# Kernel tuning notes

Hardware: AMD Instinct MI355X
Metric: run time of the kernel (lower is better)

Reference implementation:

```python
import jax, jax.numpy as jnp
import numpy as np

B, N, F, FH, H = 8, 2048, 64, 64, 4
NEG_BIG = -1e10


def setup_inputs() -> dict:
    key = jax.random.key(0)
    k_x, k_a, k_w, k_as, k_an = jax.random.split(key, 5)
    X = jax.random.normal(k_x, (B, N, F), dtype=jnp.float32)
    A = (jax.random.uniform(k_a, (B, N, N)) < 0.1).astype(jnp.float32)
    A = jnp.maximum(A, jnp.eye(N, dtype=jnp.float32)[None])
    W = jax.random.normal(k_w, (H, F, FH), dtype=jnp.float32) * (1.0 / np.sqrt(F))
    b = jnp.zeros((H, FH), dtype=jnp.float32)
    a_self = jax.random.normal(k_as, (H, FH), dtype=jnp.float32) * (1.0 / np.sqrt(FH))
    a_neigh = jax.random.normal(k_an, (H, FH), dtype=jnp.float32) * (1.0 / np.sqrt(FH))
    return {"X": X, "A": A, "W": W, "b": b, "a_self": a_self, "a_neigh": a_neigh}


def reference(X, A, W, b, a_self, a_neigh):
    # per-head linear projection: [B,H,N,FH]
    feats = jnp.einsum("bnf,hfo->bhno", X, W)
    # additive attention logits: e_ij = leaky_relu(a_s.h_i + a_n.h_j)
    s_self = jnp.einsum("bhno,ho->bhn", feats, a_self)   # [B,H,N]
    s_neigh = jnp.einsum("bhno,ho->bhn", feats, a_neigh)  # [B,H,N]
    scores = s_self[:, :, :, None] + s_neigh[:, :, None, :]  # [B,H,N,N]
    scores = jax.nn.leaky_relu(scores, negative_slope=0.2)
    scores = scores + (1.0 - A)[:, None] * NEG_BIG  # adjacency mask
    attn = jax.nn.softmax(scores, axis=-1)
    # weighted aggregation + bias (dropouts are identity at inference)
    out = jnp.einsum("bhnm,bhmo->bhno", attn, feats) + b[None, :, None, :]
    # concat heads -> [B,N,H*FH], then activation
    Bd, Hd, Nd, Fd = out.shape
    out = jnp.transpose(out, (0, 2, 1, 3)).reshape(Bd, Nd, Hd * Fd)
    return jax.nn.relu(out)
```

## Files before the change

### kernel.cpp

```cpp
#include <hip/hip_runtime.h>
#include <hip/hip_bf16.h>
#include <stdint.h>

#define B_ 8
#define N_ 2048
#define F_ 64
#define FH_ 64
#define H_ 4
#define C_ (H_*FH_)
#define CHUNK 64
#define NCHUNK (N_/CHUNK)
#define LOG2E 1.44269504088896340736f

typedef short short8 __attribute__((ext_vector_type(8)));
typedef float f32x4 __attribute__((ext_vector_type(4)));

__device__ __forceinline__ short f2bf(float f) {
    __hip_bfloat16 h = __float2bfloat16(f);
    return __builtin_bit_cast(short, h);
}

__global__ __launch_bounds__(256) void kf(const float* __restrict__ A,
                                          const float* __restrict__ X,
                                          const float* __restrict__ W,
                                          const float* __restrict__ a_self,
                                          const float* __restrict__ a_neigh,
                                          unsigned long long* __restrict__ Amask,
                                          __hip_bfloat16* __restrict__ featsT,
                                          float* __restrict__ ss,
                                          float* __restrict__ sn) {
    __shared__ float a_lds[2][FH_];
    __shared__ __hip_bfloat16 cw_lds[FH_ * 72];
    const int bx = blockIdx.x;
    const int tid = threadIdx.x;
    const int wave = tid >> 6, lane = tid & 63;

    if (bx >= 1024) {
        const int R = (bx - 1024) * 4 + wave;
        const float* arow = A + (size_t)R * N_;
        unsigned long long* mrow = Amask + (size_t)R * (N_ / 64);
#pragma unroll
        for (int i = 0; i < 8; ++i) {
            float a0 = arow[i * 256 + lane];
            float a1 = arow[i * 256 + 64 + lane];
            float a2 = arow[i * 256 + 128 + lane];
            float a3 = arow[i * 256 + 192 + lane];
            unsigned long long m0 = __ballot(a0 != 0.0f);
            unsigned long long m1 = __ballot(a1 != 0.0f);
            unsigned long long m2 = __ballot(a2 != 0.0f);
            unsigned long long m3 = __ballot(a3 != 0.0f);
            if (lane == 0) {
                mrow[i * 4 + 0] = m0; mrow[i * 4 + 1] = m1;
                mrow[i * 4 + 2] = m2; mrow[i * 4 + 3] = m3;
            }
        }
        return;
    }

    const int nb = bx & 31, h = (bx >> 5) & 3, b = bx >> 7;

    if (tid < 64)       a_lds[0][tid] = a_self[h * FH_ + tid];
    else if (tid < 128) a_lds[1][tid - 64] = a_neigh[h * FH_ + tid - 64];
    {
        int f = tid >> 2, o0 = (tid & 3) * 16;
        const float* wsrc = W + ((size_t)(h * F_ + f)) * FH_ + o0;
#pragma unroll
        for (int k = 0; k < 16; ++k)
            cw_lds[(o0 + k) * 72 + f] = __float2bfloat16(wsrc[k]);
    }
    __syncthreads();

    const int m = lane & 15, q = lane >> 4;
    const int nl = wave * 16 + m;
    const int n = nb * 64 + nl;
    f32x4 acc[4] = {};
#pragma unroll
    for (int ks = 0; ks < 2; ++ks) {
        const float* xp = X + ((size_t)(b * N_ + n)) * F_ + ks * 32 + q * 8;
        float4 x0 = *(const float4*)xp;
        float4 x1 = *(const float4*)(xp + 4);
        short8 bfrag;
        bfrag[0] = f2bf(x0.x); bfrag[1] = f2bf(x0.y);
        bfrag[2] = f2bf(x0.z); bfrag[3] = f2bf(x0.w);
        bfrag[4] = f2bf(x1.x); bfrag[5] = f2bf(x1.y);
        bfrag[6] = f2bf(x1.z); bfrag[7] = f2bf(x1.w);
#pragma unroll
        for (int ot = 0; ot < 4; ++ot) {
            short8 afrag = *(const short8*)(cw_lds + (ot * 16 + m) * 72 + ks * 32 + q * 8);
            acc[ot] = __builtin_amdgcn_mfma_f32_16x16x32_bf16(afrag, bfrag, acc[ot], 0, 0, 0);
        }
    }
    __syncthreads();
    float ssv = 0.f, snv = 0.f;
#pragma unroll
    for (int ot = 0; ot < 4; ++ot) {
#pragma unroll
        for (int r = 0; r < 4; ++r) {
            int orow = ot * 16 + q * 4 + r;
            float v = acc[ot][r];
            cw_lds[orow * 72 + nl] = __float2bfloat16(v);
            ssv += v * a_lds[0][orow];
            snv += v * a_lds[1][orow];
        }
    }
    ssv += __shfl_xor(ssv, 16); ssv += __shfl_xor(ssv, 32);
    snv += __shfl_xor(snv, 16); snv += __shfl_xor(snv, 32);
    __syncthreads();
    {
        int o = tid >> 2, c = (tid & 3) * 16;
        const __hip_bfloat16* src = cw_lds + o * 72 + c;
        __hip_bfloat16* dst = featsT + ((size_t)(b * H_ + h) * FH_ + o) * N_ + nb * 64 + c;
        *(uint4*)dst       = *(const uint4*)src;
        *(uint4*)(dst + 8) = *(const uint4*)(src + 8);
    }
    if (lane < 16) {
        size_t idx = ((size_t)(b * H_ + h)) * N_ + n;
        ss[idx] = ssv * LOG2E;
        sn[idx] = snv * LOG2E;
    }
}

__global__ __launch_bounds__(256) void k3_attn(const unsigned int* __restrict__ Amask,
                                               const __hip_bfloat16* __restrict__ featsT,
                                               const float* __restrict__ ss,
                                               const float* __restrict__ sn,
                                               const float* __restrict__ bias,
                                               float* __restrict__ out) {
    __shared__ float e1_lds[N_];
    __shared__ float e2_lds[N_];

    const int tile = blockIdx.x, h = blockIdx.y, b = blockIdx.z;
    const int tid = threadIdx.x, wave = tid >> 6, lane = tid & 63;
    const int m = lane & 15, q = lane >> 4;
    const int wavebase = tile * 128 + wave * 32;

    {
        const float4* snrow = (const float4*)(sn + ((size_t)(b * H_ + h)) * N_);
        float4* e1v = (float4*)e1_lds;
        float4* e2v = (float4*)e2_lds;
#pragma unroll
        for (int i = 0; i < 2; ++i) {
            int idx = tid + i * 256;
            float4 v = snrow[idx];
            float4 u1, u2;
            u1.x = exp2f(v.x); u1.y = exp2f(v.y); u1.z = exp2f(v.z); u1.w = exp2f(v.w);
            u2.x = exp2f(0.2f * v.x); u2.y = exp2f(0.2f * v.y);
            u2.z = exp2f(0.2f * v.z); u2.w = exp2f(0.2f * v.w);
            e1v[idx] = u1; e2v[idx] = u2;
        }
    }
    const float* ssrow = ss + ((size_t)(b * H_ + h)) * N_;
    const float ssi0 = ssrow[wavebase + m];
    const float ssi1 = ssrow[wavebase + 16 + m];
    const float e1i0 = exp2f(ssi0), e2i0 = exp2f(0.2f * ssi0);
    const float e1i1 = exp2f(ssi1), e2i1 = exp2f(0.2f * ssi1);

    const __hip_bfloat16* fhead = featsT + ((size_t)(b * H_ + h)) * FH_ * N_;
    const unsigned int* mrow0 = Amask + ((size_t)(b * N_) + wavebase + m) * (N_ / 32);
    const unsigned int* mrow1 = mrow0 + (size_t)16 * (N_ / 32);

    __syncthreads();

    f32x4 acc[2][4] = {};
    f32x4 accl[2] = {};
    short8 ones;
#pragma unroll
    for (int s = 0; s < 8; ++s) ones[s] = (short)0x3F80;

    uint2 mk0 = *(const uint2*)(mrow0);
    uint2 mk1 = *(const uint2*)(mrow1);

    for (int c = 0; c < NCHUNK; ++c) {
        const int cg = c * CHUNK;
        short8 fA[4], fB[4];
#pragma unroll
        for (int ct = 0; ct < 4; ++ct) {
            const __hip_bfloat16* fp = fhead + (size_t)(ct * 16 + m) * N_ + cg + q * 8;
            fA[ct] = *(const short8*)fp;
            fB[ct] = *(const short8*)(fp + 32);
        }
        uint2 mk0n = mk0, mk1n = mk1;
        if (c + 1 < NCHUNK) {
            mk0n = *(const uint2*)(mrow0 + (c + 1) * 2);
            mk1n = *(const uint2*)(mrow1 + (c + 1) * 2);
        }

        float4 eA10 = *(const float4*)(e1_lds + cg + q * 8);
        float4 eA11 = *(const float4*)(e1_lds + cg + q * 8 + 4);
        float4 eB10 = *(const float4*)(e1_lds + cg + 32 + q * 8);
        float4 eB11 = *(const float4*)(e1_lds + cg + 32 + q * 8 + 4);
        float4 eA20 = *(const float4*)(e2_lds + cg + q * 8);
        float4 eA21 = *(const float4*)(e2_lds + cg + q * 8 + 4);
        float4 eB20 = *(const float4*)(e2_lds + cg + 32 + q * 8);
        float4 eB21 = *(const float4*)(e2_lds + cg + 32 + q * 8 + 4);
        float e1A[8] = {eA10.x, eA10.y, eA10.z, eA10.w, eA11.x, eA11.y, eA11.z, eA11.w};
        float e1B[8] = {eB10.x, eB10.y, eB10.z, eB10.w, eB11.x, eB11.y, eB11.z, eB11.w};
        float e2A[8] = {eA20.x, eA20.y, eA20.z, eA20.w, eA21.x, eA21.y, eA21.z, eA21.w};
        float e2B[8] = {eB20.x, eB20.y, eB20.z, eB20.w, eB21.x, eB21.y, eB21.z, eB21.w};

        short8 p0A, p0B, p1A, p1B;
#pragma unroll
        for (int s = 0; s < 8; ++s) {
            float vA0 = fmaxf(e1i0 * e1A[s], e2i0 * e2A[s]);
            float vB0 = fmaxf(e1i0 * e1B[s], e2i0 * e2B[s]);
            float vA1 = fmaxf(e1i1 * e1A[s], e2i1 * e2A[s]);
            float vB1 = fmaxf(e1i1 * e1B[s], e2i1 * e2B[s]);
            const int bit = q * 8 + s;
            p0A[s] = (mk0.x >> bit) & 1 ? f2bf(vA0) : (short)0;
            p0B[s] = (mk0.y >> bit) & 1 ? f2bf(vB0) : (short)0;
            p1A[s] = (mk1.x >> bit) & 1 ? f2bf(vA1) : (short)0;
            p1B[s] = (mk1.y >> bit) & 1 ? f2bf(vB1) : (short)0;
        }
#pragma unroll
        for (int ct = 0; ct < 4; ++ct) {
            acc[0][ct] = __builtin_amdgcn_mfma_f32_16x16x32_bf16(p0A, fA[ct], acc[0][ct], 0, 0, 0);
            acc[0][ct] = __builtin_amdgcn_mfma_f32_16x16x32_bf16(p0B, fB[ct], acc[0][ct], 0, 0, 0);
            acc[1][ct] = __builtin_amdgcn_mfma_f32_16x16x32_bf16(p1A, fA[ct], acc[1][ct], 0, 0, 0);
            acc[1][ct] = __builtin_amdgcn_mfma_f32_16x16x32_bf16(p1B, fB[ct], acc[1][ct], 0, 0, 0);
        }
        accl[0] = __builtin_amdgcn_mfma_f32_16x16x32_bf16(p0A, ones, accl[0], 0, 0, 0);
        accl[0] = __builtin_amdgcn_mfma_f32_16x16x32_bf16(p0B, ones, accl[0], 0, 0, 0);
        accl[1] = __builtin_amdgcn_mfma_f32_16x16x32_bf16(p1A, ones, accl[1], 0, 0, 0);
        accl[1] = __builtin_amdgcn_mfma_f32_16x16x32_bf16(p1B, ones, accl[1], 0, 0, 0);

        mk0 = mk0n; mk1 = mk1n;
    }

    float bc[4];
#pragma unroll
    for (int ct = 0; ct < 4; ++ct) bc[ct] = bias[h * FH_ + ct * 16 + m];

#pragma unroll
    for (int g = 0; g < 2; ++g) {
#pragma unroll
        for (int r = 0; r < 4; ++r) {
            float inv = 1.0f / accl[g][r];
            int gr = wavebase + g * 16 + q * 4 + r;
#pragma unroll
            for (int ct = 0; ct < 4; ++ct) {
                float v = acc[g][ct][r] * inv + bc[ct];
                out[((size_t)(b * N_) + gr) * C_ + h * FH_ + ct * 16 + m] = fmaxf(v, 0.0f);
            }
        }
    }
}

extern "C" void kernel_launch(void* const* d_in, const int* in_sizes, int n_in,
                              void* d_out, int out_size, void* d_ws, size_t ws_size,
                              hipStream_t stream) {
    const float* X       = (const float*)d_in[0];
    const float* A       = (const float*)d_in[1];
    const float* W       = (const float*)d_in[2];
    const float* bias    = (const float*)d_in[3];
    const float* a_self  = (const float*)d_in[4];
    const float* a_neigh = (const float*)d_in[5];
    float* out = (float*)d_out;

    char* ws = (char*)d_ws;
    __hip_bfloat16* featsT = (__hip_bfloat16*)(ws);
    float* ss              = (float*)(ws + 8421376);
    float* sn              = (float*)(ws + 8683520);
    unsigned long long* Am = (unsigned long long*)(ws + 8945664);

    kf      <<<5120, 256, 0, stream>>>(A, X, W, a_self, a_neigh, Am, featsT, ss, sn);
    k3_attn <<<dim3(N_ / 128, H_, B_), 256, 0, stream>>>((const unsigned int*)Am, featsT, ss, sn, bias, out);
}
```

Measured before the change: 282.7 us.

## Halve rows per wave in attention kernel and remap blocks for XCD locality

Each wave now handles 16 query rows instead of 32, so the attention grid doubles from 512 to 1024 blocks, and launch bounds ask for 4 blocks per SM. A 1D block index is remapped so that the blocks for a given (batch, head) land on the same XCD (index mod 8) and share its L2 for featsT and the mask. The aim is more parallelism and occupancy, plus better cache reuse. The cost is that each block recomputes the exp2 tables for the whole row into LDS and reads featsT per 16 rows rather than 32, which doubles that traffic.

```diff
diff --git a/kernel.cpp b/kernel.cpp
--- a/kernel.cpp
+++ b/kernel.cpp
@@ -120,19 +120,25 @@
     }
 }
 
-__global__ __launch_bounds__(256) void k3_attn(const unsigned int* __restrict__ Amask,
-                                               const __hip_bfloat16* __restrict__ featsT,
-                                               const float* __restrict__ ss,
-                                               const float* __restrict__ sn,
-                                               const float* __restrict__ bias,
-                                               float* __restrict__ out) {
+__global__ __launch_bounds__(256, 4) void k3_attn(const unsigned int* __restrict__ Amask,
+                                                  const __hip_bfloat16* __restrict__ featsT,
+                                                  const float* __restrict__ ss,
+                                                  const float* __restrict__ sn,
+                                                  const float* __restrict__ bias,
+                                                  float* __restrict__ out) {
     __shared__ float e1_lds[N_];
     __shared__ float e2_lds[N_];
 
-    const int tile = blockIdx.x, h = blockIdx.y, b = blockIdx.z;
+    const int L = blockIdx.x;
+    const int g = L & 7;
+    const int s = L >> 3;
+    const int bh = g * 4 + (s >> 5);
+    const int tile = s & 31;
+    const int b = bh >> 2, h = bh & 3;
+
     const int tid = threadIdx.x, wave = tid >> 6, lane = tid & 63;
     const int m = lane & 15, q = lane >> 4;
-    const int wavebase = tile * 128 + wave * 32;
+    const int wavebase = tile * 64 + wave * 16;
 
     {
         const float4* snrow = (const float4*)(sn + ((size_t)(b * H_ + h)) * N_);
@@ -149,26 +155,21 @@
             e1v[idx] = u1; e2v[idx] = u2;
         }
     }
-    const float* ssrow = ss + ((size_t)(b * H_ + h)) * N_;
-    const float ssi0 = ssrow[wavebase + m];
-    const float ssi1 = ssrow[wavebase + 16 + m];
-    const float e1i0 = exp2f(ssi0), e2i0 = exp2f(0.2f * ssi0);
-    const float e1i1 = exp2f(ssi1), e2i1 = exp2f(0.2f * ssi1);
+    const float ssi = ss[((size_t)(b * H_ + h)) * N_ + wavebase + m];
+    const float e1i = exp2f(ssi), e2i = exp2f(0.2f * ssi);
 
     const __hip_bfloat16* fhead = featsT + ((size_t)(b * H_ + h)) * FH_ * N_;
-    const unsigned int* mrow0 = Amask + ((size_t)(b * N_) + wavebase + m) * (N_ / 32);
-    const unsigned int* mrow1 = mrow0 + (size_t)16 * (N_ / 32);
-
-    __syncthreads();
-
-    f32x4 acc[2][4] = {};
-    f32x4 accl[2] = {};
+    const unsigned int* mrow = Amask + ((size_t)(b * N_) + wavebase + m) * (N_ / 32);
+
+    __syncthreads();
+
+    f32x4 acc[4] = {};
+    f32x4 accl = {};
     short8 ones;
 #pragma unroll
-    for (int s = 0; s < 8; ++s) ones[s] = (short)0x3F80;
-
-    uint2 mk0 = *(const uint2*)(mrow0);
-    uint2 mk1 = *(const uint2*)(mrow1);
+    for (int ss_ = 0; ss_ < 8; ++ss_) ones[ss_] = (short)0x3F80;
+
+    uint2 mk = *(const uint2*)(mrow);
 
     for (int c = 0; c < NCHUNK; ++c) {
         const int cg = c * CHUNK;
@@ -179,11 +180,8 @@
             fA[ct] = *(const short8*)fp;
             fB[ct] = *(const short8*)(fp + 32);
         }
-        uint2 mk0n = mk0, mk1n = mk1;
-        if (c + 1 < NCHUNK) {
-            mk0n = *(const uint2*)(mrow0 + (c + 1) * 2);
-            mk1n = *(const uint2*)(mrow1 + (c + 1) * 2);
-        }
+        uint2 mkn = mk;
+        if (c + 1 < NCHUNK) mkn = *(const uint2*)(mrow + (c + 1) * 2);
 
         float4 eA10 = *(const float4*)(e1_lds + cg + q * 8);
         float4 eA11 = *(const float4*)(e1_lds + cg + q * 8 + 4);
@@ -198,32 +196,24 @@
         float e2A[8] = {eA20.x, eA20.y, eA20.z, eA20.w, eA21.x, eA21.y, eA21.z, eA21.w};
         float e2B[8] = {eB20.x, eB20.y, eB20.z, eB20.w, eB21.x, eB21.y, eB21.z, eB21.w};
 
-        short8 p0A, p0B, p1A, p1B;
-#pragma unroll
-        for (int s = 0; s < 8; ++s) {
-            float vA0 = fmaxf(e1i0 * e1A[s], e2i0 * e2A[s]);
-            float vB0 = fmaxf(e1i0 * e1B[s], e2i0 * e2B[s]);
-            float vA1 = fmaxf(e1i1 * e1A[s], e2i1 * e2A[s]);
-            float vB1 = fmaxf(e1i1 * e1B[s], e2i1 * e2B[s]);
-            const int bit = q * 8 + s;
-            p0A[s] = (mk0.x >> bit) & 1 ? f2bf(vA0) : (short)0;
-            p0B[s] = (mk0.y >> bit) & 1 ? f2bf(vB0) : (short)0;
-            p1A[s] = (mk1.x >> bit) & 1 ? f2bf(vA1) : (short)0;
-            p1B[s] = (mk1.y >> bit) & 1 ? f2bf(vB1) : (short)0;
+        short8 pA, pB;
+#pragma unroll
+        for (int t = 0; t < 8; ++t) {
+            float vA = fmaxf(e1i * e1A[t], e2i * e2A[t]);
+            float vB = fmaxf(e1i * e1B[t], e2i * e2B[t]);
+            const int bit = q * 8 + t;
+            pA[t] = (mk.x >> bit) & 1 ? f2bf(vA) : (short)0;
+            pB[t] = (mk.y >> bit) & 1 ? f2bf(vB) : (short)0;
         }
 #pragma unroll
         for (int ct = 0; ct < 4; ++ct) {
-            acc[0][ct] = __builtin_amdgcn_mfma_f32_16x16x32_bf16(p0A, fA[ct], acc[0][ct], 0, 0, 0);
-            acc[0][ct] = __builtin_amdgcn_mfma_f32_16x16x32_bf16(p0B, fB[ct], acc[0][ct], 0, 0, 0);
-            acc[1][ct] = __builtin_amdgcn_mfma_f32_16x16x32_bf16(p1A, fA[ct], acc[1][ct], 0, 0, 0);
-            acc[1][ct] = __builtin_amdgcn_mfma_f32_16x16x32_bf16(p1B, fB[ct], acc[1][ct], 0, 0, 0);
-        }
-        accl[0] = __builtin_amdgcn_mfma_f32_16x16x32_bf16(p0A, ones, accl[0], 0, 0, 0);
-        accl[0] = __builtin_amdgcn_mfma_f32_16x16x32_bf16(p0B, ones, accl[0], 0, 0, 0);
-        accl[1] = __builtin_amdgcn_mfma_f32_16x16x32_bf16(p1A, ones, accl[1], 0, 0, 0);
-        accl[1] = __builtin_amdgcn_mfma_f32_16x16x32_bf16(p1B, ones, accl[1], 0, 0, 0);
-
-        mk0 = mk0n; mk1 = mk1n;
+            acc[ct] = __builtin_amdgcn_mfma_f32_16x16x32_bf16(pA, fA[ct], acc[ct], 0, 0, 0);
+            acc[ct] = __builtin_amdgcn_mfma_f32_16x16x32_bf16(pB, fB[ct], acc[ct], 0, 0, 0);
+        }
+        accl = __builtin_amdgcn_mfma_f32_16x16x32_bf16(pA, ones, accl, 0, 0, 0);
+        accl = __builtin_amdgcn_mfma_f32_16x16x32_bf16(pB, ones, accl, 0, 0, 0);
+
+        mk = mkn;
     }
 
     float bc[4];
@@ -231,16 +221,13 @@
     for (int ct = 0; ct < 4; ++ct) bc[ct] = bias[h * FH_ + ct * 16 + m];
 
 #pragma unroll
-    for (int g = 0; g < 2; ++g) {
-#pragma unroll
-        for (int r = 0; r < 4; ++r) {
-            float inv = 1.0f / accl[g][r];
-            int gr = wavebase + g * 16 + q * 4 + r;
-#pragma unroll
-            for (int ct = 0; ct < 4; ++ct) {
-                float v = acc[g][ct][r] * inv + bc[ct];
-                out[((size_t)(b * N_) + gr) * C_ + h * FH_ + ct * 16 + m] = fmaxf(v, 0.0f);
-            }
+    for (int r = 0; r < 4; ++r) {
+        float inv = 1.0f / accl[r];
+        int gr = wavebase + q * 4 + r;
+#pragma unroll
+        for (int ct = 0; ct < 4; ++ct) {
+            float v = acc[ct][r] * inv + bc[ct];
+            out[((size_t)(b * N_) + gr) * C_ + h * FH_ + ct * 16 + m] = fmaxf(v, 0.0f);
         }
     }
 }
@@ -263,5 +250,5 @@
     unsigned long long* Am = (unsigned long long*)(ws + 8945664);
 
     kf      <<<5120, 256, 0, stream>>>(A, X, W, a_self, a_neigh, Am, featsT, ss, sn);
-    k3_attn <<<dim3(N_ / 128, H_, B_), 256, 0, stream>>>((const unsigned int*)Am, featsT, ss, sn, bias, out);
-}
+    k3_attn <<<1024, 256, 0, stream>>>((const unsigned int*)Am, featsT, ss, sn, bias, out);
+}
```

After: 338.0 us. +19.6%, slower.
